# Kernel tuning notes

Measured on AMD Instinct MI355X. Metric: run time of the kernel, lower is better.

## Reference

```python
import jax, jax.numpy as jnp
import numpy as np

B, H, W = 4, 240, 320
J = 2            # BONE_NUM
F = 64           # FEATURE_CHANNELS
R = 32           # voxel RESOLUTION
THRESH = 0.7
BIG = 1e30
# channel layout from init_hp(): nocs | mask | loc | pose | skin | conf | feature
NE = 3
ME = NE + 1
LE = ME + J * 3
PE = LE + J * 3
SE = PE + J + 2
CE = SE + J
FE = CE + F      # = 86 total channels


def _rodrigues(r):
    # axis-angle [..., 3] -> rotation matrix [..., 3, 3]
    ang = jnp.sqrt(jnp.sum(r * r, -1, keepdims=True)) + 1e-8
    ax = r / ang
    x, y, z = ax[..., 0], ax[..., 1], ax[..., 2]
    zz = jnp.zeros_like(x)
    K = jnp.stack([zz, -z, y, z, zz, -x, -y, x, zz], -1).reshape(r.shape[:-1] + (3, 3))
    c = jnp.cos(ang)[..., None]
    s = jnp.sin(ang)[..., None]
    return jnp.eye(3, dtype=r.dtype) + s * K + (1.0 - c) * (K @ K)


def setup_inputs() -> dict:
    key = jax.random.key(0)
    return {"output": jax.random.normal(key, (B, FE, H, W), dtype=jnp.float32)}


def _forward(output):
    mask = jax.nn.sigmoid(output[:, NE])                      # [B,H,W]
    conf = output[:, SE:CE]                                   # [B,J,H,W]
    score = jax.nn.sigmoid(conf) * mask[:, None]
    score = score / (score.reshape(B, J, -1).sum(-1)[:, :, None, None] + 1e-5)

    def vote(jmap):  # weighted joint voting, joint map detached as in torch
        jm = jmap.reshape(B, J, 3, H, W) * mask[:, None, None]
        jm = jax.lax.stop_gradient(jm) * score[:, :, None]
        return jm.reshape(B, J, 3, -1).sum(-1)                # [B,J,3]

    loc = vote(output[:, ME:LE])
    rot = vote(output[:, LE:PE])
    # pad root joint (identity transform) at index 0 -> J+1 joints
    locp = jnp.concatenate([jnp.zeros((B, 1, 3), output.dtype), loc], 1)
    rotp = jnp.concatenate([jnp.zeros((B, 1, 3), output.dtype), rot], 1)
    Rm = _rodrigues(-rotp)                                    # [B,J+1,3,3]
    t = locp[..., None]
    trans = t - Rm @ t                                        # Trans(loc)@Rot@Trans(-loc)
    bottom = jnp.broadcast_to(jnp.array([0, 0, 0, 1], output.dtype), (B, J + 1, 1, 4))
    M = jnp.concatenate([jnp.concatenate([Rm, trans], -1), bottom], -2)  # [B,J+1,4,4]

    # per-pixel hard segmentation one-hot over flags 1..J+1 (flag 0 -> zero transform)
    seg = output[:, PE:SE]                                    # [B,J+2,H,W]
    amax = jnp.argmax(seg, axis=1)                            # [B,H,W]
    oh = (amax[:, None] == jnp.arange(1, J + 2)[None, :, None, None]).astype(output.dtype)
    T = jnp.einsum('bjhw,bjpq->bhwpq', oh, M)                 # [B,H,W,4,4]

    nocs = jnp.moveaxis(output[:, :NE], 1, -1)                # [B,H,W,3]
    homog = jnp.concatenate([nocs, jnp.ones_like(nocs[..., :1])], -1)
    pn = jnp.einsum('bhwpq,bhwq->bhwp', T[..., :3, :], homog) # reposed points [B,H,W,3]

    masked = mask > THRESH
    m4 = masked[..., None]
    low = jnp.where(m4, pn, BIG).min(axis=(1, 2))             # [B,3]
    up = jnp.where(m4, pn, -BIG).max(axis=(1, 2))
    scale = (up - low).max(-1)                                # [B]
    safe = jnp.where(scale == 0, 1.0, scale)[:, None, None, None]
    pn_n = jnp.where((scale != 0)[:, None, None, None], (pn - low[:, None, None]) / safe, pn)
    pn_map = jnp.where(m4, pn_n, 0.0)                         # [B,H,W,3]

    out_cat = jnp.concatenate([output, jnp.moveaxis(pn_map, -1, 1)], axis=1)

    # lift + discretize: scatter per-pixel features of valid points into R^3 grid
    feat = jnp.moveaxis(output[:, CE:FE], 1, -1)              # [B,H,W,F]
    vx = jnp.clip(jnp.floor(pn_map * R).astype(jnp.int32), 0, R - 1)
    flat = vx[..., 0] * R * R + vx[..., 1] * R + vx[..., 2]
    flat = jnp.where(masked, flat, R ** 3)                    # invalid -> dump bin

    def scat(fl, ft):
        g = jnp.zeros((R ** 3 + 1, F), ft.dtype).at[fl.reshape(-1)].add(ft.reshape(-1, F))
        return jnp.moveaxis(g[:R ** 3].reshape(R, R, R, F), -1, 0)

    occ = jax.vmap(scat)(flat, feat)                          # [B,F,R,R,R]
    return out_cat, occ


def reference(output):
    return _forward(output)
```

## Files before the change

kernel.cpp:

```cpp
#include <hip/hip_runtime.h>
#include <math.h>

#define HW     76800
#define HW4    19200
#define NCH    86
#define OCH    89
#define NB     4
#define VOX    32768
#define NBLKV  75
#define THRESHF 0.7f
#define BIGF   1e30f

typedef float f4 __attribute__((ext_vector_type(4)));


__device__ __forceinline__ float sigmoidf_(float x) {
    if (x >= 0.f) { return 1.f / (1.f + expf(-x)); }
    float e = expf(x); return e / (1.f + e);
}
__device__ __forceinline__ unsigned fkey(float f) {
    unsigned u = __float_as_uint(f);
    return (u & 0x80000000u) ? ~u : (u | 0x80000000u);
}
__device__ __forceinline__ float funkey(unsigned k) {
    unsigned u = (k & 0x80000000u) ? (k ^ 0x80000000u) : ~k;
    return __uint_as_float(u);
}
__device__ __forceinline__ int vox1(float q) {
    int v = (int)floorf(q * 32.f);
    return v < 0 ? 0 : (v > 31 ? 31 : v);
}

__global__ __launch_bounds__(256) void k_votes_zero(const f4* __restrict__ in4,
                                                    float* __restrict__ ws,
                                                    f4* __restrict__ zp, unsigned n4) {
    const int b = blockIdx.y, bx = blockIdx.x;
    const int tid = threadIdx.x;
    {
        unsigned gid = ((unsigned)(b * NBLKV + bx)) * 256u + tid;
        f4 z = {0.f, 0.f, 0.f, 0.f};
        for (unsigned i = gid; i < n4; i += NB * NBLKV * 256u)
            __builtin_nontemporal_store(z, &zp[i]);
    }
    if (b == 0 && bx == 0 && tid < 24) {
        unsigned* keys = (unsigned*)(ws + 256);
        keys[tid] = ((tid % 6) < 3) ? fkey(BIGF) : fkey(-BIGF);
    }
    const size_t ib = (size_t)b * NCH * HW4 + bx * 256 + tid;
    f4 mv = in4[ib + (size_t)3 * HW4];
    f4 c0 = in4[ib + (size_t)20 * HW4];
    f4 c1 = in4[ib + (size_t)21 * HW4];
    f4 L[12];
#pragma unroll
    for (int i = 0; i < 12; i++) L[i] = in4[ib + (size_t)(4 + i) * HW4];
    float acc[14];
#pragma unroll
    for (int i = 0; i < 14; i++) acc[i] = 0.f;
#pragma unroll
    for (int k = 0; k < 4; k++) {
        float m  = sigmoidf_(mv[k]);
        float s0 = sigmoidf_(c0[k]) * m;
        float s1 = sigmoidf_(c1[k]) * m;
        float w0 = m * s0, w1 = m * s1;
        acc[0] += s0; acc[7] += s1;
#pragma unroll
        for (int c = 0; c < 3; c++) {
            acc[1 + c]  += L[c][k]     * w0;
            acc[8 + c]  += L[3 + c][k] * w1;
            acc[4 + c]  += L[6 + c][k] * w0;
            acc[11 + c] += L[9 + c][k] * w1;
        }
    }
    __shared__ float red[4][14];
    int lane = tid & 63, wid = tid >> 6;
#pragma unroll
    for (int i = 0; i < 14; i++) {
        float v = acc[i];
        for (int off = 32; off > 0; off >>= 1) v += __shfl_down(v, off, 64);
        if (lane == 0) red[wid][i] = v;
    }
    __syncthreads();
    if (tid < 14)
        ws[512 + (b * NBLKV + bx) * 16 + tid] =
            red[0][tid] + red[1][tid] + red[2][tid] + red[3][tid];
}

__global__ __launch_bounds__(256) void k_minmax(const f4* __restrict__ in4,
                                                float* __restrict__ ws) {
    __shared__ float vsh[14];
    __shared__ float Msh[36];
    const int b = blockIdx.y, bx = blockIdx.x, tid = threadIdx.x;
    if (tid < 14) {
        const float* part = ws + 512 + (size_t)b * NBLKV * 16 + tid;
        float s = 0.f;
#pragma unroll 5
        for (int blk = 0; blk < NBLKV; blk++) s += part[blk * 16];
        vsh[tid] = s;
    }
    __syncthreads();
    if (tid < 3) {
        int k = tid;
        float lp0 = 0, lp1 = 0, lp2 = 0, rp0 = 0, rp1 = 0, rp2 = 0;
        if (k > 0) {
            const float* v = vsh + (k - 1) * 7;
            float d = v[0] + 1e-5f;
            lp0 = v[1] / d; lp1 = v[2] / d; lp2 = v[3] / d;
            rp0 = v[4] / d; rp1 = v[5] / d; rp2 = v[6] / d;
        }
        float rx = -rp0, ry = -rp1, rz = -rp2;
        float ang = sqrtf(rx * rx + ry * ry + rz * rz) + 1e-8f;
        float ax = rx / ang, ay = ry / ang, az = rz / ang;
        float K[3][3] = {{0.f, -az, ay}, {az, 0.f, -ax}, {-ay, ax, 0.f}};
        float c = cosf(ang), s = sinf(ang);
        float K2[3][3], Rm[3][3];
#pragma unroll
        for (int i = 0; i < 3; i++)
#pragma unroll
            for (int j = 0; j < 3; j++)
                K2[i][j] = K[i][0] * K[0][j] + K[i][1] * K[1][j] + K[i][2] * K[2][j];
#pragma unroll
        for (int i = 0; i < 3; i++)
#pragma unroll
            for (int j = 0; j < 3; j++)
                Rm[i][j] = (i == j ? 1.f : 0.f) + s * K[i][j] + (1.f - c) * K2[i][j];
#pragma unroll
        for (int i = 0; i < 3; i++) {
            float tt = (i == 0 ? lp0 : (i == 1 ? lp1 : lp2));
            float tr = tt - (Rm[i][0] * lp0 + Rm[i][1] * lp1 + Rm[i][2] * lp2);
            Msh[k * 12 + i * 4 + 0] = Rm[i][0];
            Msh[k * 12 + i * 4 + 1] = Rm[i][1];
            Msh[k * 12 + i * 4 + 2] = Rm[i][2];
            Msh[k * 12 + i * 4 + 3] = tr;
            if (bx == 0) {
                float* M = ws + 64 + (b * 3 + k) * 12;
                M[i * 4 + 0] = Rm[i][0]; M[i * 4 + 1] = Rm[i][1];
                M[i * 4 + 2] = Rm[i][2]; M[i * 4 + 3] = tr;
            }
        }
    }
    __syncthreads();

    const size_t ib = (size_t)b * NCH * HW4 + bx * 256 + tid;
    f4 n0 = in4[ib], n1 = in4[ib + HW4], n2 = in4[ib + 2 * HW4];
    f4 mv = in4[ib + 3 * HW4];
    f4 g0 = in4[ib + 16 * HW4], g1 = in4[ib + 17 * HW4];
    f4 g2 = in4[ib + 18 * HW4], g3 = in4[ib + 19 * HW4];
    float mn[3] = {BIGF, BIGF, BIGF}, mx[3] = {-BIGF, -BIGF, -BIGF};
#pragma unroll
    for (int k = 0; k < 4; k++) {
        float m = sigmoidf_(mv[k]);
        if (!(m > THRESHF)) continue;
        int am = 0; float bb = g0[k];
        if (g1[k] > bb) { bb = g1[k]; am = 1; }
        if (g2[k] > bb) { bb = g2[k]; am = 2; }
        if (g3[k] > bb) { bb = g3[k]; am = 3; }
        float px = 0.f, py = 0.f, pz = 0.f;
        if (am > 0) {
            const float* Mk = Msh + (am - 1) * 12;
            float a = n0[k], bq = n1[k], cq = n2[k];
            px = Mk[0] * a + Mk[1] * bq + Mk[2]  * cq + Mk[3];
            py = Mk[4] * a + Mk[5] * bq + Mk[6]  * cq + Mk[7];
            pz = Mk[8] * a + Mk[9] * bq + Mk[10] * cq + Mk[11];
        }
        mn[0] = fminf(mn[0], px); mn[1] = fminf(mn[1], py); mn[2] = fminf(mn[2], pz);
        mx[0] = fmaxf(mx[0], px); mx[1] = fmaxf(mx[1], py); mx[2] = fmaxf(mx[2], pz);
    }
    __shared__ float rmn[4][3], rmx[4][3];
    int lane = tid & 63, wid = tid >> 6;
#pragma unroll
    for (int i = 0; i < 3; i++) {
        float v = mn[i];
        for (int off = 32; off > 0; off >>= 1) v = fminf(v, __shfl_down(v, off, 64));
        if (lane == 0) rmn[wid][i] = v;
        float u = mx[i];
        for (int off = 32; off > 0; off >>= 1) u = fmaxf(u, __shfl_down(u, off, 64));
        if (lane == 0) rmx[wid][i] = u;
    }
    __syncthreads();
    unsigned* keys = (unsigned*)(ws + 256);
    if (tid < 3) {
        float v = fminf(fminf(rmn[0][tid], rmn[1][tid]), fminf(rmn[2][tid], rmn[3][tid]));
        atomicMin(&keys[b * 6 + tid], fkey(v));
    } else if (tid < 6) {
        int i = tid - 3;
        float v = fmaxf(fmaxf(rmx[0][i], rmx[1][i]), fmaxf(rmx[2][i], rmx[3][i]));
        atomicMax(&keys[b * 6 + 3 + i], fkey(v));
    }
}

template<bool VOXMAJOR>
__global__ __launch_bounds__(256) void k_scatter(const f4* __restrict__ in4,
                                                 f4* __restrict__ out4,
                                                 float* __restrict__ dst,
                                                 const float* __restrict__ ws) {
    __shared__ float tile[64][257];
    __shared__ float accz[4][64];
    const int b = blockIdx.y, blk = blockIdx.x;
    const int tid = threadIdx.x, lane = tid & 63, w = tid >> 6;
    const size_t ib4 = (size_t)b * NCH * HW4 + (size_t)blk * 64;
    const size_t ob4 = (size_t)b * OCH * HW4 + (size_t)blk * 64;

    const unsigned* keys = (const unsigned*)(ws + 256);
    float l0 = funkey(keys[b * 6 + 0]), l1 = funkey(keys[b * 6 + 1]), l2 = funkey(keys[b * 6 + 2]);
    float u0 = funkey(keys[b * 6 + 3]), u1 = funkey(keys[b * 6 + 4]), u2 = funkey(keys[b * 6 + 5]);
    float scale = fmaxf(u0 - l0, fmaxf(u1 - l1, u2 - l2));
    float safe = (scale == 0.f) ? 1.f : scale;
    bool flag = scale != 0.f;
    float z0 = flag ? (0.f - l0) / safe : 0.f;
    float z1 = flag ? (0.f - l1) / safe : 0.f;
    float z2 = flag ? (0.f - l2) / safe : 0.f;
    const int fl0 = vox1(z0) * 1024 + vox1(z1) * 32 + vox1(z2);

    const float* ibs = (const float*)in4 + (size_t)b * NCH * HW + blk * 256 + tid;
    float* obs = (float*)out4 + (size_t)b * OCH * HW + blk * 256 + tid;
    float n0 = ibs[0], n1 = ibs[(size_t)HW], n2 = ibs[(size_t)2 * HW];
    float mvv = ibs[(size_t)3 * HW];
    float g0 = ibs[(size_t)16 * HW], g1 = ibs[(size_t)17 * HW];
    float g2 = ibs[(size_t)18 * HW], g3 = ibs[(size_t)19 * HW];
    float m = sigmoidf_(mvv);
    bool masked = m > THRESHF;
    int am = 0;
    { float bb = g0;
      if (g1 > bb) { bb = g1; am = 1; }
      if (g2 > bb) { bb = g2; am = 2; }
      if (g3 > bb) { bb = g3; am = 3; } }
    bool glb  = masked && (am != 0);
    bool spec = masked && (am == 0);
    float px = 0.f, py = 0.f, pz = 0.f;
    if (am > 0) {
        const float* Mk = ws + 64 + b * 36 + (am - 1) * 12;
        px = Mk[0] * n0 + Mk[1] * n1 + Mk[2]  * n2 + Mk[3];
        py = Mk[4] * n0 + Mk[5] * n1 + Mk[6]  * n2 + Mk[7];
        pz = Mk[8] * n0 + Mk[9] * n1 + Mk[10] * n2 + Mk[11];
    }
    float qx, qy, qz;
    if (flag) { qx = (px - l0) / safe; qy = (py - l1) / safe; qz = (pz - l2) / safe; }
    else      { qx = px; qy = py; qz = pz; }
    float ox = masked ? qx : 0.f, oy = masked ? qy : 0.f, oz = masked ? qz : 0.f;
    obs[(size_t)86 * HW] = ox;
    obs[(size_t)87 * HW] = oy;
    obs[(size_t)88 * HW] = oz;
    int flat = glb ? (vox1(ox) * 1024 + vox1(oy) * 32 + vox1(oz)) : fl0;
    unsigned long long gm = __ballot(glb);
    unsigned long long sm = __ballot(spec);

#pragma unroll
    for (int i = 0; i < 6; i++) {
        int c = w + 4 * i;
        if (c < 22) {
            f4 v = in4[ib4 + (size_t)c * HW4 + lane];
            out4[ob4 + (size_t)c * HW4 + lane] = v;
        }
    }
#pragma unroll
    for (int i = 0; i < 16; i++) {
        int c = w * 16 + i;
        f4 v = in4[ib4 + (size_t)(22 + c) * HW4 + lane];
        out4[ob4 + (size_t)(22 + c) * HW4 + lane] = v;
        tile[c][4 * lane + 0] = v[0]; tile[c][4 * lane + 1] = v[1];
        tile[c][4 * lane + 2] = v[2]; tile[c][4 * lane + 3] = v[3];
    }
    __syncthreads();

    while (gm) {
        int i0 = __ffsll(gm) - 1;
        int fl = __shfl(flat, i0, 64);
        unsigned long long match = __ballot(flat == fl) & gm;
        gm &= ~match;
        float s = 0.f;
        unsigned long long mm = match;
        while (mm) {
            int j = __ffsll(mm) - 1; mm &= mm - 1;
            s += tile[lane][w * 64 + j];
        }
        if (VOXMAJOR)
            atomicAdd(&dst[(((size_t)b * VOX + fl) << 6) + lane], s);
        else
            atomicAdd(&dst[(((size_t)(b * 64 + lane)) << 15) + fl], s);
    }
    float sacc = 0.f;
    while (sm) {
        int j = __ffsll(sm) - 1; sm &= sm - 1;
        sacc += tile[lane][w * 64 + j];
    }
    accz[w][lane] = sacc;
    __syncthreads();
    if (tid < 64) {
        float s = accz[0][tid] + accz[1][tid] + accz[2][tid] + accz[3][tid];
        if (s != 0.f) {
            if (VOXMAJOR)
                atomicAdd(&dst[(((size_t)b * VOX + fl0) << 6) + tid], s);
            else
                atomicAdd(&dst[(((size_t)(b * 64 + tid)) << 15) + fl0], s);
        }
    }
}

__global__ __launch_bounds__(256) void k_transpose(const float* __restrict__ tmp,
                                                   float* __restrict__ occ) {
    __shared__ float ld[64][65];
    const int b = blockIdx.y;
    const int vox0 = blockIdx.x * 64;
    const int t = threadIdx.x;
    const int v = t & 63, g = t >> 6;
    const float* src = tmp + (((size_t)b * VOX + vox0 + v) << 6) + g * 16;
#pragma unroll
    for (int i = 0; i < 4; i++) {
        f4 x = *(const f4*)(src + 4 * i);
        ld[g * 16 + 4 * i + 0][v] = x[0];
        ld[g * 16 + 4 * i + 1][v] = x[1];
        ld[g * 16 + 4 * i + 2][v] = x[2];
        ld[g * 16 + 4 * i + 3][v] = x[3];
    }
    __syncthreads();
    const int f = t >> 2;
    float* dstp = occ + (((size_t)(b * 64 + f)) << 15) + vox0;
#pragma unroll
    for (int i = 0; i < 4; i++) {
        int mq = (t & 3) * 4 + i;
        f4 x;
        x[0] = ld[f][4 * mq + 0]; x[1] = ld[f][4 * mq + 1];
        x[2] = ld[f][4 * mq + 2]; x[3] = ld[f][4 * mq + 3];
        *(f4*)(dstp + 4 * mq) = x;
    }
}

extern "C" void kernel_launch(void* const* d_in, const int* in_sizes, int n_in,
                              void* d_out, int out_size, void* d_ws, size_t ws_size,
                              hipStream_t stream) {
    const f4* in4 = (const f4*)d_in[0];
    float* out = (float*)d_out;
    float* ws = (float*)d_ws;
    float* occ = out + (size_t)NB * OCH * HW;
    float* tmp = ws + 32768;
    const size_t tmp_bytes = (size_t)NB * VOX * 64 * sizeof(float);
    const bool voxmajor = ws_size >= 32768 * sizeof(float) + tmp_bytes;
    const unsigned n4 = (unsigned)(tmp_bytes / 16);

    dim3 g75(NBLKV, NB);
    if (voxmajor) k_votes_zero<<<g75, 256, 0, stream>>>(in4, ws, (f4*)tmp, n4);
    else          k_votes_zero<<<g75, 256, 0, stream>>>(in4, ws, (f4*)occ, n4);
    k_minmax<<<g75, 256, 0, stream>>>(in4, ws);
    dim3 gs(300, NB);
    if (voxmajor) {
        k_scatter<true><<<gs, 256, 0, stream>>>(in4, (f4*)out, tmp, ws);
        dim3 gt(VOX / 64, NB);
        k_transpose<<<gt, 256, 0, stream>>>(tmp, occ);
    } else {
        k_scatter<false><<<gs, 256, 0, stream>>>(in4, (f4*)out, occ, ws);
    }
}
```

Before: 103.4 us.

## Track dirty voxels in a bitmap and skip untouched blocks in transpose

Scatter now sets a per-voxel occupancy bit in a workspace bitmap whenever it adds into the voxel-major temp buffer. The transpose kernel checks the bitmap and, for 64-voxel blocks with no hits, writes zeros directly instead of reading the temp buffer. The zeroing work in the votes kernel is split into separate extra blocks, which also clear the bitmap. This aims to cut global read traffic on the large temp buffer, at the cost of extra atomicOr operations in scatter.

After: 101.1 us, median of 2. 2.2% less time.

```diff
diff --git a/kernel.cpp b/kernel.cpp
--- a/kernel.cpp
+++ b/kernel.cpp
@@ -36,16 +36,21 @@
                                                     f4* __restrict__ zp, unsigned n4) {
     const int b = blockIdx.y, bx = blockIdx.x;
     const int tid = threadIdx.x;
-    {
-        unsigned gid = ((unsigned)(b * NBLKV + bx)) * 256u + tid;
+
+    if (bx >= NBLKV) {
+        const int zb = b * NBLKV + (bx - NBLKV);
+        unsigned gid = (unsigned)zb * 256u + tid;
         f4 z = {0.f, 0.f, 0.f, 0.f};
         for (unsigned i = gid; i < n4; i += NB * NBLKV * 256u)
             __builtin_nontemporal_store(z, &zp[i]);
-    }
-    if (b == 0 && bx == 0 && tid < 24) {
-        unsigned* keys = (unsigned*)(ws + 256);
-        keys[tid] = ((tid % 6) < 3) ? fkey(BIGF) : fkey(-BIGF);
-    }
+        if (gid < NB * 1024) ((unsigned*)(ws + 8192))[gid] = 0u;
+        if (zb == 0 && tid < 24) {
+            unsigned* keys = (unsigned*)(ws + 256);
+            keys[tid] = ((tid % 6) < 3) ? fkey(BIGF) : fkey(-BIGF);
+        }
+        return;
+    }
+
     const size_t ib = (size_t)b * NCH * HW4 + bx * 256 + tid;
     f4 mv = in4[ib + (size_t)3 * HW4];
     f4 c0 = in4[ib + (size_t)20 * HW4];
@@ -192,13 +197,14 @@
 __global__ __launch_bounds__(256) void k_scatter(const f4* __restrict__ in4,
                                                  f4* __restrict__ out4,
                                                  float* __restrict__ dst,
-                                                 const float* __restrict__ ws) {
+                                                 float* __restrict__ ws) {
     __shared__ float tile[64][257];
     __shared__ float accz[4][64];
     const int b = blockIdx.y, blk = blockIdx.x;
     const int tid = threadIdx.x, lane = tid & 63, w = tid >> 6;
     const size_t ib4 = (size_t)b * NCH * HW4 + (size_t)blk * 64;
     const size_t ob4 = (size_t)b * OCH * HW4 + (size_t)blk * 64;
+    unsigned* bm = (unsigned*)(ws + 8192) + b * 1024;
 
     const unsigned* keys = (const unsigned*)(ws + 256);
     float l0 = funkey(keys[b * 6 + 0]), l1 = funkey(keys[b * 6 + 1]), l2 = funkey(keys[b * 6 + 2]);
@@ -260,6 +266,8 @@
         tile[c][4 * lane + 0] = v[0]; tile[c][4 * lane + 1] = v[1];
         tile[c][4 * lane + 2] = v[2]; tile[c][4 * lane + 3] = v[3];
     }
+    if (VOXMAJOR && tid == 0 && sm)
+        atomicOr(&bm[fl0 >> 5], 1u << (fl0 & 31));
     __syncthreads();
 
     while (gm) {
@@ -273,10 +281,12 @@
             int j = __ffsll(mm) - 1; mm &= mm - 1;
             s += tile[lane][w * 64 + j];
         }
-        if (VOXMAJOR)
+        if (VOXMAJOR) {
+            if (lane == 0) atomicOr(&bm[fl >> 5], 1u << (fl & 31));
             atomicAdd(&dst[(((size_t)b * VOX + fl) << 6) + lane], s);
-        else
+        } else {
             atomicAdd(&dst[(((size_t)(b * 64 + lane)) << 15) + fl], s);
+        }
     }
     float sacc = 0.f;
     while (sm) {
@@ -297,11 +307,24 @@
 }
 
 __global__ __launch_bounds__(256) void k_transpose(const float* __restrict__ tmp,
-                                                   float* __restrict__ occ) {
+                                                   float* __restrict__ occ,
+                                                   const float* __restrict__ ws) {
     __shared__ float ld[64][65];
     const int b = blockIdx.y;
     const int vox0 = blockIdx.x * 64;
     const int t = threadIdx.x;
+    const unsigned* bm = (const unsigned*)(ws + 8192) + b * 1024;
+    const unsigned dirty = bm[vox0 >> 5] | bm[(vox0 >> 5) + 1];
+    const int f = t >> 2, sub = t & 3;
+    float* dstp = occ + (((size_t)(b * 64 + f)) << 15) + vox0;
+
+    if (dirty == 0u) {
+        f4 z = {0.f, 0.f, 0.f, 0.f};
+#pragma unroll
+        for (int i = 0; i < 4; i++)
+            *(f4*)(dstp + 4 * (sub * 4 + i)) = z;
+        return;
+    }
     const int v = t & 63, g = t >> 6;
     const float* src = tmp + (((size_t)b * VOX + vox0 + v) << 6) + g * 16;
 #pragma unroll
@@ -313,11 +336,9 @@
         ld[g * 16 + 4 * i + 3][v] = x[3];
     }
     __syncthreads();
-    const int f = t >> 2;
-    float* dstp = occ + (((size_t)(b * 64 + f)) << 15) + vox0;
 #pragma unroll
     for (int i = 0; i < 4; i++) {
-        int mq = (t & 3) * 4 + i;
+        int mq = sub * 4 + i;
         f4 x;
         x[0] = ld[f][4 * mq + 0]; x[1] = ld[f][4 * mq + 1];
         x[2] = ld[f][4 * mq + 2]; x[3] = ld[f][4 * mq + 3];
@@ -337,15 +358,16 @@
     const bool voxmajor = ws_size >= 32768 * sizeof(float) + tmp_bytes;
     const unsigned n4 = (unsigned)(tmp_bytes / 16);
 
+    dim3 gv(NBLKV * 2, NB);
+    if (voxmajor) k_votes_zero<<<gv, 256, 0, stream>>>(in4, ws, (f4*)tmp, n4);
+    else          k_votes_zero<<<gv, 256, 0, stream>>>(in4, ws, (f4*)occ, n4);
     dim3 g75(NBLKV, NB);
-    if (voxmajor) k_votes_zero<<<g75, 256, 0, stream>>>(in4, ws, (f4*)tmp, n4);
-    else          k_votes_zero<<<g75, 256, 0, stream>>>(in4, ws, (f4*)occ, n4);
     k_minmax<<<g75, 256, 0, stream>>>(in4, ws);
     dim3 gs(300, NB);
     if (voxmajor) {
         k_scatter<true><<<gs, 256, 0, stream>>>(in4, (f4*)out, tmp, ws);
         dim3 gt(VOX / 64, NB);
-        k_transpose<<<gt, 256, 0, stream>>>(tmp, occ);
+        k_transpose<<<gt, 256, 0, stream>>>(tmp, occ, ws);
     } else {
         k_scatter<false><<<gs, 256, 0, stream>>>(in4, (f4*)out, occ, ws);
     }
```
